# Performance work log

Measured on AMD Instinct MI355X. Metric: run time of the kernel, lower is better.

## Reference

```python
import jax, jax.numpy as jnp
import numpy as np


def _time_encoding(t, hidden_dim):
    # Sinusoidal continuous-time encoding: t [B,T] -> [B,T,H]
    half = hidden_dim // 2
    freqs = jnp.exp(-jnp.arange(half, dtype=t.dtype) * (np.log(10000.0) / half))
    ang = t[..., None] * freqs  # [B,T,half]
    return jnp.concatenate([jnp.sin(ang), jnp.cos(ang)], axis=-1)


def _gru(x_tbh, w_ih, w_hh, b_ih, b_hh):
    # PyTorch-convention GRU over time-major input [T,B,H]
    B = x_tbh.shape[1]
    H = w_hh.shape[1]
    h0 = jnp.zeros((B, H), x_tbh.dtype)

    def step(h, x):
        gi = x @ w_ih.T + b_ih
        gh = h @ w_hh.T + b_hh
        i_r, i_z, i_n = jnp.split(gi, 3, axis=-1)
        h_r, h_z, h_n = jnp.split(gh, 3, axis=-1)
        r = jax.nn.sigmoid(i_r + h_r)
        z = jax.nn.sigmoid(i_z + h_z)
        n = jnp.tanh(i_n + r * h_n)
        h_new = (1.0 - z) * n + z * h
        return h_new, h_new

    _, ys = jax.lax.scan(step, h0, x_tbh)
    return ys  # [T,B,H]


def setup_inputs():
    key = jax.random.key(0)
    ks = jax.random.split(key, 8)
    B, T, D, H = 32, 256, 64, 128
    x = jax.random.normal(ks[0], (B, T, D), jnp.float32)
    missing_mask = (jax.random.uniform(ks[1], (B, T, D)) < 0.5).astype(jnp.float32)
    visit_time = jnp.cumsum(jax.random.uniform(ks[2], (B, T), jnp.float32) * 2.0, axis=1)
    time_delta = jnp.zeros((B, T), jnp.float32)
    lengths = jax.random.randint(ks[3], (B,), T // 2, T + 1).astype(jnp.int32)
    lengths = lengths.at[0].set(T)  # pad_packed returns max(lengths) steps; pin to T
    sensor_embed = jax.random.normal(ks[4], (D, H), jnp.float32) * 0.02
    k = 1.0 / np.sqrt(H)
    gru_w_ih = jax.random.uniform(ks[5], (3 * H, H), jnp.float32, -k, k)
    gru_w_hh = jax.random.uniform(ks[6], (3 * H, H), jnp.float32, -k, k)
    gru_b_ih = jax.random.uniform(ks[7], (3 * H,), jnp.float32, -k, k)
    gru_b_hh = jnp.zeros((3 * H,), jnp.float32)
    return dict(x=x, missing_mask=missing_mask, visit_time=visit_time,
                time_delta=time_delta, lengths=lengths, sensor_embed=sensor_embed,
                gru_w_ih=gru_w_ih, gru_w_hh=gru_w_hh, gru_b_ih=gru_b_ih, gru_b_hh=gru_b_hh)


def reference(x, missing_mask, visit_time, time_delta, lengths, sensor_embed,
              gru_w_ih, gru_w_hh, gru_b_ih, gru_b_hh):
    B, T, D = x.shape
    H = sensor_embed.shape[1]
    observed = 1.0 - missing_mask                                   # [B,T,D]
    # sensor tokens: per-(t,sensor) embedding scaled by value, zeroed if missing
    sensor_tokens = x[..., None] * sensor_embed[None, None] * observed[..., None]  # [B,T,D,H]
    presence = observed.mean(axis=1)                                # [B,D]
    sim = jax.nn.relu(sensor_embed @ sensor_embed.T)                # [D,D]
    adj = presence[:, :, None] * presence[:, None, :] * sim[None]   # [B,D,D]
    adj = adj + jnp.eye(D, dtype=x.dtype)[None]
    adj = adj / jnp.maximum(adj.sum(axis=-1, keepdims=True), 1e-6)
    graph_tokens = jnp.einsum('bij,btjh->btih', adj, sensor_tokens) # [B,T,D,H]
    visit_repr = graph_tokens.mean(axis=2) + _time_encoding(visit_time, H)  # [B,T,H]
    # dropout is identity in eval mode
    ys = _gru(jnp.swapaxes(visit_repr, 0, 1), gru_w_ih, gru_w_hh, gru_b_ih, gru_b_hh)
    out = jnp.swapaxes(ys, 0, 1)                                    # [B,T,H]
    # pad_packed_sequence semantics: zeros beyond each sequence length
    mask = (jnp.arange(T)[None, :] < lengths[:, None])[..., None]
    return out * mask
```

## Files before the change

kernel.cpp:

```cpp
#include <hip/hip_runtime.h>
#include <hip/hip_bf16.h>

#define B_ 32
#define T_ 256
#define D_ 64
#define H_ 128
#define G_ 384

typedef _Float16 half8 __attribute__((ext_vector_type(8)));
typedef _Float16 half4v __attribute__((ext_vector_type(4)));
typedef float float4v __attribute__((ext_vector_type(4)));
typedef int int8v __attribute__((ext_vector_type(8)));

__device__ __forceinline__ float fsigmoid2(float s){
  return __builtin_amdgcn_rcpf(1.0f + __builtin_amdgcn_exp2f(-s));
}
__device__ __forceinline__ float ftanh2(float t){
  return 1.0f - 2.0f*__builtin_amdgcn_rcpf(1.0f + __builtin_amdgcn_exp2f(t));
}
#define LOG2E  1.442695041f
#define LOG2E2 2.885390082f

#define BAR() do{ asm volatile("s_waitcnt lgkmcnt(0)" ::: "memory"); \
                  __builtin_amdgcn_s_barrier(); \
                  asm volatile("" ::: "memory"); } while(0)

__global__ void __launch_bounds__(256) adj_k(const float* mm, const float* E,
                                             float* wcol){
  int b = blockIdx.x;
  int tid = threadIdx.x;
  int d = tid & 63, q = tid >> 6;
  __shared__ float spp[4][64];
  __shared__ float sp[64];
  __shared__ float sE[64*129];
  __shared__ float ssim[64*65];
  __shared__ float srs[64];
  float p = 0.0f;
  for (int t = q*64; t < q*64+64; t++) p += 1.0f - mm[(b*T_ + t)*D_ + d];
  spp[q][d] = p;
  for (int i = tid; i < D_*H_; i += 256){ int r = i >> 7, c = i & 127; sE[r*129+c] = E[i]; }
  __syncthreads();
  if (tid < 64) sp[tid] = (spp[0][tid]+spp[1][tid]+spp[2][tid]+spp[3][tid]) * (1.0f/T_);
  __syncthreads();
  float rowE[128];
  #pragma unroll
  for (int k = 0; k < 128; k++) rowE[k] = sE[d*129+k];
  for (int i = q*16; i < q*16+16; i++){
    float s = 0.0f;
    #pragma unroll
    for (int k = 0; k < 128; k++) s += rowE[k]*sE[i*129+k];
    ssim[d*65+i] = fmaxf(s, 0.0f);
  }
  __syncthreads();
  if (tid < 64){
    float rs = 0.0f;
    for (int j = 0; j < 64; j++) rs += sp[j]*ssim[tid*65+j];
    srs[tid] = fmaxf(sp[tid]*rs + 1.0f, 1e-6f);
  }
  __syncthreads();
  if (tid < 64){
    float s = 0.0f;
    for (int i = 0; i < 64; i++) s += sp[i]*ssim[tid*65+i]/srs[i];
    wcol[b*64 + tid] = sp[tid]*s + 1.0f/srs[tid];
  }
}

#define AVP 72
#define VRP 136
#define SEP 132
__global__ void __launch_bounds__(512,1) gi_k(const float* x, const float* mm,
                                              const float* vt, const float* E,
                                              const float* wih, const float* bih,
                                              const float* bhh, const float* wcol,
                                              _Float16* gi3){
  int bid = blockIdx.x;
  int b = bid >> 3, t0 = (bid & 7)*32;
  int tid = threadIdx.x;
  int w = tid >> 6, l = tid & 63;
  int lq = l >> 4, lm = l & 15;

  __shared__ __align__(16) _Float16 av[32*AVP];
  __shared__ __align__(16) _Float16 vrA[32*VRP];
  __shared__ __align__(16) _Float16 sEl[64*SEP];
  __shared__ float sVt[32];

  {
    int i = tid*4, t = i >> 6, d4 = i & 63;
    long src = (long)(b*T_ + t0 + t)*D_ + d4;
    float4 xv = *(const float4*)&x[src];
    float4 mv = *(const float4*)&mm[src];
    float4 wv = *(const float4*)&wcol[b*D_ + d4];
    half4v h;
    h[0]=(_Float16)(xv.x*(1.0f-mv.x)*wv.x*(1.0f/64));
    h[1]=(_Float16)(xv.y*(1.0f-mv.y)*wv.y*(1.0f/64));
    h[2]=(_Float16)(xv.z*(1.0f-mv.z)*wv.z*(1.0f/64));
    h[3]=(_Float16)(xv.w*(1.0f-mv.w)*wv.w*(1.0f/64));
    *(half4v*)&av[t*AVP + d4] = h;
  }
  {
    int r = tid >> 3, c0 = (tid & 7)*16;
    #pragma unroll
    for (int g = 0; g < 4; g++){
      float4 v = *(const float4*)&E[r*H_ + c0 + g*4];
      half4v h;
      h[0]=(_Float16)v.x; h[1]=(_Float16)v.y; h[2]=(_Float16)v.z; h[3]=(_Float16)v.w;
      *(half4v*)&sEl[r*SEP + c0 + g*4] = h;
    }
  }
  if (tid < 32) sVt[tid] = vt[b*T_ + t0 + tid];
  __syncthreads();

  half8 bE[2];
  #pragma unroll
  for (int kc = 0; kc < 2; kc++){
    half8 f;
    #pragma unroll
    for (int jj = 0; jj < 8; jj++)
      f[jj] = sEl[(kc*32 + lq*8 + jj)*SEP + 16*w + lm];
    bE[kc] = f;
  }

  float4v accA[2] = {{0,0,0,0},{0,0,0,0}};
  #pragma unroll
  for (int kc = 0; kc < 2; kc++){
    #pragma unroll
    for (int mt = 0; mt < 2; mt++){
      half8 a = *(const half8*)&av[(mt*16+lm)*AVP + kc*32 + lq*8];
      accA[mt] = __builtin_amdgcn_mfma_f32_16x16x32_f16(a, bE[kc], accA[mt], 0,0,0);
    }
  }
  {
    int h = 16*w + lm;
    float fr = __expf(-(float)(h & 63) * 0.14391157f);
    #pragma unroll
    for (int mt = 0; mt < 2; mt++){
      #pragma unroll
      for (int r = 0; r < 4; r++){
        int tl = mt*16 + lq*4 + r;
        float ang = sVt[tl] * fr;
        float e = (h < 64) ? __sinf(ang) : __cosf(ang);
        vrA[tl*VRP + h] = (_Float16)(accA[mt][r] + e);
      }
    }
  }
  __syncthreads();

  half8 bW[3][4]; float biW[3];
  #pragma unroll
  for (int q = 0; q < 3; q++){
    int g = 16*(3*w + q) + lm;
    float sc = (g < 2*H_) ? LOG2E : LOG2E2;
    biW[q] = (bih[g] + (g < 2*H_ ? bhh[g] : 0.0f)) * sc;
    #pragma unroll
    for (int kc = 0; kc < 4; kc++){
      const float* src = &wih[(long)g*H_ + kc*32 + lq*8];
      float4 x0 = *(const float4*)src;
      float4 x1 = *(const float4*)(src+4);
      half8 f;
      f[0]=(_Float16)(x0.x*sc); f[1]=(_Float16)(x0.y*sc); f[2]=(_Float16)(x0.z*sc); f[3]=(_Float16)(x0.w*sc);
      f[4]=(_Float16)(x1.x*sc); f[5]=(_Float16)(x1.y*sc); f[6]=(_Float16)(x1.z*sc); f[7]=(_Float16)(x1.w*sc);
      bW[q][kc] = f;
    }
  }
  float4v cB[2][3];
  #pragma unroll
  for (int mt = 0; mt < 2; mt++)
    #pragma unroll
    for (int q = 0; q < 3; q++) cB[mt][q] = (float4v){0,0,0,0};
  #pragma unroll
  for (int kc = 0; kc < 4; kc++){
    #pragma unroll
    for (int mt = 0; mt < 2; mt++){
      half8 a = *(const half8*)&vrA[(mt*16+lm)*VRP + kc*32 + lq*8];
      #pragma unroll
      for (int q = 0; q < 3; q++)
        cB[mt][q] = __builtin_amdgcn_mfma_f32_16x16x32_f16(a, bW[q][kc], cB[mt][q], 0,0,0);
    }
  }
  #pragma unroll
  for (int mt = 0; mt < 2; mt++){
    #pragma unroll
    for (int q = 0; q < 3; q++){
      int g = 16*(3*w + q) + lm;
      int tb = t0 + mt*16 + lq*4;
      half4v hv;
      hv[0]=(_Float16)(cB[mt][q][0] + biW[q]); hv[1]=(_Float16)(cB[mt][q][1] + biW[q]);
      hv[2]=(_Float16)(cB[mt][q][2] + biW[q]); hv[3]=(_Float16)(cB[mt][q][3] + biW[q]);
      *(half4v*)&gi3[((long)(b*G_ + g))*T_ + tb] = hv;
    }
  }
}

__global__ void __attribute__((amdgpu_waves_per_eu(2, 2)))
__launch_bounds__(512) gru_k(const _Float16* gi3, const float* whh,
                             const float* bhh, const int* lengths,
                             float* out){
  int b = blockIdx.x;
  int tid = threadIdx.x;
  int w = tid >> 6, l = tid & 63;
  int lq = l >> 4;
  int j = 16*w + (l & 15);
  bool gate = (l < 16);
  int len = lengths[b];

  __shared__ __align__(32) unsigned char hb8[2][H_];

  int8v bf8[3];
  #pragma unroll
  for (int q = 0; q < 3; q++){
    int row = q*H_ + 16*w + (l & 15);
    float sc16 = ((q == 2) ? LOG2E2 : LOG2E) * 16.0f;
    const float* src = &whh[(long)row*H_ + lq*32];
    int8v f;
    #pragma unroll
    for (int d = 0; d < 8; d++){
      float4 v = *(const float4*)(src + d*4);
      int pk = __builtin_amdgcn_cvt_pk_fp8_f32(v.x*sc16, v.y*sc16, 0, false);
      pk = __builtin_amdgcn_cvt_pk_fp8_f32(v.z*sc16, v.w*sc16, pk, true);
      f[d] = pk;
    }
    bf8[q] = f;
  }
  float bn_ = bhh[2*H_ + j] * LOG2E2;
  const _Float16* pr = gi3 + ((long)b*G_ + j)*T_;
  const _Float16* pz = pr + (long)H_*T_;
  const _Float16* pn = pr + (long)2*H_*T_;

  if (tid < H_){ hb8[0][tid] = 0; hb8[1][tid] = 0; }

  half8 prA, pzA, pnA, prB, pzB, pnB;
  prA = *(const half8*)pr; pzA = *(const half8*)pz; pnA = *(const half8*)pn;
  __syncthreads();

  float hval = 0.0f;

  auto substeps = [&](half8 cr, half8 cz, half8 cn, int c){
    float ho[8];
    #pragma unroll
    for (int i = 0; i < 8; i++){
      const int rp = i & 1;
      int8v av = *(const int8v*)&hb8[rp][lq*32];
      float4v c0 = {0,0,0,0}, c1 = {0,0,0,0}, c2 = {0,0,0,0};
      __builtin_amdgcn_s_setprio(1);
      c0 = __builtin_amdgcn_mfma_scale_f32_16x16x128_f8f6f4(av, bf8[0], c0, 0, 0, 0, 123, 0, 123);
      c1 = __builtin_amdgcn_mfma_scale_f32_16x16x128_f8f6f4(av, bf8[1], c1, 0, 0, 0, 123, 0, 123);
      c2 = __builtin_amdgcn_mfma_scale_f32_16x16x128_f8f6f4(av, bf8[2], c2, 0, 0, 0, 123, 0, 123);
      __builtin_amdgcn_s_setprio(0);
      float r = fsigmoid2((float)cr[i] + c0[0]);
      float z = fsigmoid2((float)cz[i] + c1[0]);
      float n = ftanh2((float)cn[i] + r*(c2[0] + bn_));
      hval = (1.0f - z)*n + z*hval;
      if (gate){
        int hq = __builtin_amdgcn_cvt_pk_fp8_f32(hval*16.0f, hval*16.0f, 0, false);
        hb8[rp^1][j] = (unsigned char)(hq & 0xff);
        ho[i] = (c*8 + i < len) ? hval : 0.0f;
      }
      BAR();
    }
    if (gate){
      long ob = ((long)b*T_ + c*8)*H_ + j;
      #pragma unroll
      for (int i = 0; i < 8; i++) out[ob + (long)i*H_] = ho[i];
    }
  };

  for (int c = 0; c < 32; c += 2){
    {
      int nb = (c+1)*8;
      prB = *(const half8*)(pr+nb); pzB = *(const half8*)(pz+nb); pnB = *(const half8*)(pn+nb);
    }
    substeps(prA, pzA, pnA, c);
    if (c+2 < 32){
      int nb = (c+2)*8;
      prA = *(const half8*)(pr+nb); pzA = *(const half8*)(pz+nb); pnA = *(const half8*)(pn+nb);
    }
    substeps(prB, pzB, pnB, c+1);
  }
}

extern "C" void kernel_launch(void* const* d_in, const int* in_sizes, int n_in,
                              void* d_out, int out_size, void* d_ws, size_t ws_size,
                              hipStream_t stream) {
  char* base = (char*)d_ws;
  size_t off = 0;
  auto alloc = [&](size_t bytes)->void*{
    void* p = base + off; off = (off + bytes + 255) & ~(size_t)255; return p;
  };
  float*     wcol = (float*)alloc((size_t)B_*D_*4);
  _Float16*  gi3  = (_Float16*)alloc((size_t)B_*G_*T_*2);
  if (off > ws_size) return;

  const float* x   = (const float*)d_in[0];
  const float* mm  = (const float*)d_in[1];
  const float* vt  = (const float*)d_in[2];
  const int*   len = (const int*)d_in[4];
  const float* E   = (const float*)d_in[5];
  const float* wih = (const float*)d_in[6];
  const float* whh = (const float*)d_in[7];
  const float* bih = (const float*)d_in[8];
  const float* bhh = (const float*)d_in[9];

  adj_k<<<dim3(B_),dim3(256),0,stream>>>(mm, E, wcol);
  gi_k<<<dim3(256),dim3(512),0,stream>>>(x, mm, vt, E, wih, bih, bhh, wcol, gi3);
  gru_k<<<dim3(B_),dim3(512),0,stream>>>(gi3, whh, bhh, len, (float*)d_out);
}
```

Measured before the change: 215.2 us.

## Halve GRU block to 4 waves, each computing two 16-column hidden tiles

The recurrent GRU kernel now runs 256 threads (4 waves) per batch element instead of 512, and each wave handles 32 hidden units with six fp8 MFMAs per step instead of three. The goal is to make the per-timestep barrier cheaper by synchronising fewer waves, and to give each wave independent MFMA chains it can overlap. In exchange each wave carries twice the serial MFMA and activation work on the critical path and needs more registers for weights and prefetched gate inputs.

```diff
diff --git a/kernel.cpp b/kernel.cpp
--- a/kernel.cpp
+++ b/kernel.cpp
@@ -191,90 +191,118 @@
   }
 }
 
-__global__ void __attribute__((amdgpu_waves_per_eu(2, 2)))
-__launch_bounds__(512) gru_k(const _Float16* gi3, const float* whh,
+__global__ void __attribute__((amdgpu_waves_per_eu(1, 1)))
+__launch_bounds__(256) gru_k(const _Float16* gi3, const float* whh,
                              const float* bhh, const int* lengths,
                              float* out){
   int b = blockIdx.x;
   int tid = threadIdx.x;
   int w = tid >> 6, l = tid & 63;
-  int lq = l >> 4;
-  int j = 16*w + (l & 15);
+  int lq = l >> 4, lm = l & 15;
+  int j0 = 32*w + lm;
+  int j1 = j0 + 16;
   bool gate = (l < 16);
   int len = lengths[b];
 
   __shared__ __align__(32) unsigned char hb8[2][H_];
 
-  int8v bf8[3];
+  int8v bf8[3][2];
   #pragma unroll
   for (int q = 0; q < 3; q++){
-    int row = q*H_ + 16*w + (l & 15);
     float sc16 = ((q == 2) ? LOG2E2 : LOG2E) * 16.0f;
-    const float* src = &whh[(long)row*H_ + lq*32];
-    int8v f;
-    #pragma unroll
-    for (int d = 0; d < 8; d++){
-      float4 v = *(const float4*)(src + d*4);
-      int pk = __builtin_amdgcn_cvt_pk_fp8_f32(v.x*sc16, v.y*sc16, 0, false);
-      pk = __builtin_amdgcn_cvt_pk_fp8_f32(v.z*sc16, v.w*sc16, pk, true);
-      f[d] = pk;
-    }
-    bf8[q] = f;
-  }
-  float bn_ = bhh[2*H_ + j] * LOG2E2;
-  const _Float16* pr = gi3 + ((long)b*G_ + j)*T_;
-  const _Float16* pz = pr + (long)H_*T_;
-  const _Float16* pn = pr + (long)2*H_*T_;
+    #pragma unroll
+    for (int t = 0; t < 2; t++){
+      int row = q*H_ + 32*w + t*16 + lm;
+      const float* src = &whh[(long)row*H_ + lq*32];
+      int8v f;
+      #pragma unroll
+      for (int d = 0; d < 8; d++){
+        float4 v = *(const float4*)(src + d*4);
+        int pk = __builtin_amdgcn_cvt_pk_fp8_f32(v.x*sc16, v.y*sc16, 0, false);
+        pk = __builtin_amdgcn_cvt_pk_fp8_f32(v.z*sc16, v.w*sc16, pk, true);
+        f[d] = pk;
+      }
+      bf8[q][t] = f;
+    }
+  }
+  float bn0 = bhh[2*H_ + j0] * LOG2E2;
+  float bn1 = bhh[2*H_ + j1] * LOG2E2;
+  const _Float16* pr0 = gi3 + ((long)b*G_ + j0)*T_;
+  const _Float16* pz0 = pr0 + (long)H_*T_;
+  const _Float16* pn0 = pr0 + (long)2*H_*T_;
+  const _Float16* pr1 = gi3 + ((long)b*G_ + j1)*T_;
+  const _Float16* pz1 = pr1 + (long)H_*T_;
+  const _Float16* pn1 = pr1 + (long)2*H_*T_;
 
   if (tid < H_){ hb8[0][tid] = 0; hb8[1][tid] = 0; }
 
-  half8 prA, pzA, pnA, prB, pzB, pnB;
-  prA = *(const half8*)pr; pzA = *(const half8*)pz; pnA = *(const half8*)pn;
-  __syncthreads();
-
-  float hval = 0.0f;
-
-  auto substeps = [&](half8 cr, half8 cz, half8 cn, int c){
-    float ho[8];
+  half8 prA0, pzA0, pnA0, prB0, pzB0, pnB0;
+  half8 prA1, pzA1, pnA1, prB1, pzB1, pnB1;
+  prA0 = *(const half8*)pr0; pzA0 = *(const half8*)pz0; pnA0 = *(const half8*)pn0;
+  prA1 = *(const half8*)pr1; pzA1 = *(const half8*)pz1; pnA1 = *(const half8*)pn1;
+  __syncthreads();
+
+  float hv0 = 0.0f, hv1 = 0.0f;
+
+  auto substeps = [&](half8 cr0, half8 cz0, half8 cn0,
+                      half8 cr1, half8 cz1, half8 cn1, int c){
+    float ho0[8], ho1[8];
     #pragma unroll
     for (int i = 0; i < 8; i++){
       const int rp = i & 1;
       int8v av = *(const int8v*)&hb8[rp][lq*32];
-      float4v c0 = {0,0,0,0}, c1 = {0,0,0,0}, c2 = {0,0,0,0};
+      float4v c0a = {0,0,0,0}, c0b = {0,0,0,0};
+      float4v c1a = {0,0,0,0}, c1b = {0,0,0,0};
+      float4v c2a = {0,0,0,0}, c2b = {0,0,0,0};
       __builtin_amdgcn_s_setprio(1);
-      c0 = __builtin_amdgcn_mfma_scale_f32_16x16x128_f8f6f4(av, bf8[0], c0, 0, 0, 0, 123, 0, 123);
-      c1 = __builtin_amdgcn_mfma_scale_f32_16x16x128_f8f6f4(av, bf8[1], c1, 0, 0, 0, 123, 0, 123);
-      c2 = __builtin_amdgcn_mfma_scale_f32_16x16x128_f8f6f4(av, bf8[2], c2, 0, 0, 0, 123, 0, 123);
+      c0a = __builtin_amdgcn_mfma_scale_f32_16x16x128_f8f6f4(av, bf8[0][0], c0a, 0, 0, 0, 123, 0, 123);
+      c0b = __builtin_amdgcn_mfma_scale_f32_16x16x128_f8f6f4(av, bf8[0][1], c0b, 0, 0, 0, 123, 0, 123);
+      c1a = __builtin_amdgcn_mfma_scale_f32_16x16x128_f8f6f4(av, bf8[1][0], c1a, 0, 0, 0, 123, 0, 123);
+      c1b = __builtin_amdgcn_mfma_scale_f32_16x16x128_f8f6f4(av, bf8[1][1], c1b, 0, 0, 0, 123, 0, 123);
+      c2a = __builtin_amdgcn_mfma_scale_f32_16x16x128_f8f6f4(av, bf8[2][0], c2a, 0, 0, 0, 123, 0, 123);
+      c2b = __builtin_amdgcn_mfma_scale_f32_16x16x128_f8f6f4(av, bf8[2][1], c2b, 0, 0, 0, 123, 0, 123);
       __builtin_amdgcn_s_setprio(0);
-      float r = fsigmoid2((float)cr[i] + c0[0]);
-      float z = fsigmoid2((float)cz[i] + c1[0]);
-      float n = ftanh2((float)cn[i] + r*(c2[0] + bn_));
-      hval = (1.0f - z)*n + z*hval;
+      float r0 = fsigmoid2((float)cr0[i] + c0a[0]);
+      float r1 = fsigmoid2((float)cr1[i] + c0b[0]);
+      float z0 = fsigmoid2((float)cz0[i] + c1a[0]);
+      float z1 = fsigmoid2((float)cz1[i] + c1b[0]);
+      float n0 = ftanh2((float)cn0[i] + r0*(c2a[0] + bn0));
+      float n1 = ftanh2((float)cn1[i] + r1*(c2b[0] + bn1));
+      hv0 = (1.0f - z0)*n0 + z0*hv0;
+      hv1 = (1.0f - z1)*n1 + z1*hv1;
       if (gate){
-        int hq = __builtin_amdgcn_cvt_pk_fp8_f32(hval*16.0f, hval*16.0f, 0, false);
-        hb8[rp^1][j] = (unsigned char)(hq & 0xff);
-        ho[i] = (c*8 + i < len) ? hval : 0.0f;
+        int hq0 = __builtin_amdgcn_cvt_pk_fp8_f32(hv0*16.0f, hv0*16.0f, 0, false);
+        int hq1 = __builtin_amdgcn_cvt_pk_fp8_f32(hv1*16.0f, hv1*16.0f, 0, false);
+        hb8[rp^1][j0] = (unsigned char)(hq0 & 0xff);
+        hb8[rp^1][j1] = (unsigned char)(hq1 & 0xff);
+        ho0[i] = (c*8 + i < len) ? hv0 : 0.0f;
+        ho1[i] = (c*8 + i < len) ? hv1 : 0.0f;
       }
       BAR();
     }
     if (gate){
-      long ob = ((long)b*T_ + c*8)*H_ + j;
+      long ob = ((long)b*T_ + c*8)*H_;
       #pragma unroll
-      for (int i = 0; i < 8; i++) out[ob + (long)i*H_] = ho[i];
+      for (int i = 0; i < 8; i++){
+        out[ob + (long)i*H_ + j0] = ho0[i];
+        out[ob + (long)i*H_ + j1] = ho1[i];
+      }
     }
   };
 
   for (int c = 0; c < 32; c += 2){
     {
       int nb = (c+1)*8;
-      prB = *(const half8*)(pr+nb); pzB = *(const half8*)(pz+nb); pnB = *(const half8*)(pn+nb);
-    }
-    substeps(prA, pzA, pnA, c);
+      prB0 = *(const half8*)(pr0+nb); pzB0 = *(const half8*)(pz0+nb); pnB0 = *(const half8*)(pn0+nb);
+      prB1 = *(const half8*)(pr1+nb); pzB1 = *(const half8*)(pz1+nb); pnB1 = *(const half8*)(pn1+nb);
+    }
+    substeps(prA0, pzA0, pnA0, prA1, pzA1, pnA1, c);
     if (c+2 < 32){
       int nb = (c+2)*8;
-      prA = *(const half8*)(pr+nb); pzA = *(const half8*)(pz+nb); pnA = *(const half8*)(pn+nb);
-    }
-    substeps(prB, pzB, pnB, c+1);
+      prA0 = *(const half8*)(pr0+nb); pzA0 = *(const half8*)(pz0+nb); pnA0 = *(const half8*)(pn0+nb);
+      prA1 = *(const half8*)(pr1+nb); pzA1 = *(const half8*)(pz1+nb); pnA1 = *(const half8*)(pn1+nb);
+    }
+    substeps(prB0, pzB0, pnB0, prB1, pzB1, pnB1, c+1);
   }
 }
 
@@ -302,5 +330,5 @@
 
   adj_k<<<dim3(B_),dim3(256),0,stream>>>(mm, E, wcol);
   gi_k<<<dim3(256),dim3(512),0,stream>>>(x, mm, vt, E, wih, bih, bhh, wcol, gi3);
-  gru_k<<<dim3(B_),dim3(512),0,stream>>>(gi3, whh, bhh, len, (float*)d_out);
-}
+  gru_k<<<dim3(B_),dim3(256),0,stream>>>(gi3, whh, bhh, len, (float*)d_out);
+}
```

After: 219.9 us. 1.02x slower.
